# Kernel optimization log

Hardware: AMD Instinct MI355X
Metric: run time of the kernel (lower is better)

Reference implementation:

```python
import jax, jax.numpy as jnp
import numpy as np

DIM = 1024
N_HEADS = 16
HEAD_DIM = DIM // N_HEADS
WINDOW = 64


def setup_inputs() -> dict:
    key = jax.random.key(0)
    k1, k2, k3 = jax.random.split(key, 3)
    B, N = 4, 8192
    x = jax.random.normal(k1, (B, N, DIM), dtype=jnp.float32)
    w_qkv = jax.random.normal(k2, (3 * DIM, DIM), dtype=jnp.float32) * (1.0 / np.sqrt(DIM))
    b_qkv = jnp.zeros((3 * DIM,), dtype=jnp.float32)
    w_proj = jax.random.normal(k3, (DIM, DIM), dtype=jnp.float32) * (1.0 / np.sqrt(DIM))
    b_proj = jnp.zeros((DIM,), dtype=jnp.float32)
    return {"x": x, "w_qkv": w_qkv, "b_qkv": b_qkv, "w_proj": w_proj, "b_proj": b_proj}


def reference(x, w_qkv, b_qkv, w_proj, b_proj):
    B, N, C = x.shape
    H, D, W = N_HEADS, HEAD_DIM, WINDOW
    # qkv projection: torch Linear => x @ W.T + b
    qkv = x @ w_qkv.T + b_qkv                      # [B, N, 3C]
    qkv = qkv.reshape(B, N, 3, H, D).transpose(2, 0, 3, 1, 4)  # [3, B, H, N, D]
    q, k, v = qkv[0], qkv[1], qkv[2]               # each [B, H, N, D]
    n_w = N // W                                    # N chosen divisible by window
    # split sequence into non-overlapping windows (block-diagonal attention)
    qw = q.reshape(B, H, n_w, W, D)
    kw = k.reshape(B, H, n_w, W, D)
    vw = v.reshape(B, H, n_w, W, D)
    scale = 1.0 / np.sqrt(D)
    attn = jnp.einsum('bhnqd,bhnkd->bhnqk', qw, kw) * scale  # [B,H,n_w,W,W]
    attn = jax.nn.softmax(attn, axis=-1)
    out = jnp.einsum('bhnqk,bhnkd->bhnqd', attn, vw)          # [B,H,n_w,W,D]
    out = out.reshape(B, H, N, D).transpose(0, 2, 1, 3).reshape(B, N, C)
    return out @ w_proj.T + b_proj
```

## Files before the change

### kernel.cpp

```cpp
#include <hip/hip_runtime.h>
#include <hip/hip_bf16.h>
#include <cstdint>
#include <cstddef>


typedef __attribute__((ext_vector_type(8))) short short8;
typedef __attribute__((ext_vector_type(4))) float float4v;

static __device__ __forceinline__ void async16(void* lds_p, const void* g) {
  __builtin_amdgcn_global_load_lds((const __attribute__((address_space(1))) void*)g,
                                   (__attribute__((address_space(3))) void*)lds_p,
                                   16, 0, 0);
}

static __device__ __forceinline__ unsigned short f2bf_bits(float x) {
  unsigned int u = __float_as_uint(x);
  unsigned int r = (u + 0x7fffu + ((u >> 16) & 1u)) >> 16;
  return (unsigned short)r;
}

#define S_BARRIER() asm volatile("s_barrier" ::: "memory")
#define WAIT_VM(n)  asm volatile("s_waitcnt vmcnt(" #n ")" ::: "memory")

__global__ __launch_bounds__(256) void cast_f32_to_bf16(
    const float* __restrict__ in, unsigned short* __restrict__ out, int n4) {
  int i = blockIdx.x * 256 + threadIdx.x;
  if (i >= n4) return;
  float4 v = ((const float4*)in)[i];
  ushort4 o;
  o.x = f2bf_bits(v.x); o.y = f2bf_bits(v.y);
  o.z = f2bf_bits(v.z); o.w = f2bf_bits(v.w);
  ((ushort4*)out)[i] = o;
}

template<bool OUT_BF16>
__global__ __launch_bounds__(512, 2) void gemm256(
    const unsigned short* __restrict__ A,
    const unsigned short* __restrict__ B,
    const float* __restrict__ bias,
    void* __restrict__ Cout,
    int M, int N, int K, int ntiles)
{
  extern __shared__ unsigned short lds[];

  const int t    = threadIdx.x;
  const int wave = t >> 6;
  const int lane = t & 63;
  const int lr   = lane & 15;
  const int lq   = lane >> 4;
  const int wm   = wave >> 2;
  const int wn   = wave & 3;

  const int nwg  = gridDim.x;
  const int q8   = nwg >> 3;
  const int wg   = ((int)blockIdx.x & 7) * q8 + ((int)blockIdx.x >> 3);
  const int GM   = 8;
  const int group = wg / (GM * ntiles);
  const int inG   = wg % (GM * ntiles);
  const int bm    = group * GM + (inG % GM);
  const int bn    = inG / GM;

  const int srow = t >> 3;
  const int sswz = ((t & 7) ^ (srow & 7)) << 3;
  const unsigned short* Abase = A + (size_t)(bm * 256 + srow) * K + sswz;
  const unsigned short* Bbase = B + (size_t)(bn * 256 + srow) * K + sswz;
  const int ldsw = wave * 512;

  auto stageA = [&](int kt, int c) {
    async16(lds + (kt & 1) * 16384 + c * 4096 + ldsw,
            Abase + (size_t)(c * 64) * K + kt * 64);
  };
  auto stageB = [&](int kt, int c) {
    async16(lds + 32768 + (kt & 1) * 16384 + c * 4096 + ldsw,
            Bbase + (size_t)(c * 64) * K + kt * 64);
  };

  const int g0 = ((0 + lq) ^ (lr & 7)) << 3;
  const int g1 = ((4 + lq) ^ (lr & 7)) << 3;
  const int arow0 = (wm * 128 + lr) * 64;
  const int brow0 = (wn * 64 + lr) * 64;

  float4v acc[8][4];
  #pragma unroll
  for (int i = 0; i < 8; ++i)
    #pragma unroll
    for (int j = 0; j < 4; ++j) acc[i][j] = (float4v){0.f, 0.f, 0.f, 0.f};

  const int NT = K >> 6;

  #pragma unroll
  for (int c = 0; c < 4; ++c) stageB(0, c);
  #pragma unroll
  for (int c = 0; c < 4; ++c) stageA(0, c);
  #pragma unroll
  for (int c = 0; c < 4; ++c) stageB(1, c);
  WAIT_VM(4);
  S_BARRIER();

  short8 af[4][2], bf[2][2], bf2[2][2];

  for (int kt = 0; kt < NT; ++kt) {
    const int bc = kt & 1;
    int kt1 = kt + 1; if (kt1 == NT) kt1 = 0;
    int kt2 = kt + 2; if (kt2 >= NT) kt2 -= NT;
    const unsigned short* Al = lds + bc * 16384;
    const unsigned short* Bl = lds + 32768 + bc * 16384;

    #pragma unroll
    for (int mf = 0; mf < 4; ++mf) {
      af[mf][0] = *(const short8*)(Al + arow0 + mf * 1024 + g0);
      af[mf][1] = *(const short8*)(Al + arow0 + mf * 1024 + g1);
    }
    #pragma unroll
    for (int nf = 0; nf < 2; ++nf) {
      bf[nf][0] = *(const short8*)(Bl + brow0 + nf * 1024 + g0);
      bf[nf][1] = *(const short8*)(Bl + brow0 + nf * 1024 + g1);
    }
    stageA(kt1, 0); stageA(kt1, 2);
    S_BARRIER();
    __builtin_amdgcn_s_setprio(1);
    #pragma unroll
    for (int mf = 0; mf < 4; ++mf)
      #pragma unroll
      for (int nf = 0; nf < 2; ++nf) {
        acc[mf][nf] = __builtin_amdgcn_mfma_f32_16x16x32_bf16(af[mf][0], bf[nf][0], acc[mf][nf], 0, 0, 0);
        acc[mf][nf] = __builtin_amdgcn_mfma_f32_16x16x32_bf16(af[mf][1], bf[nf][1], acc[mf][nf], 0, 0, 0);
      }
    __builtin_amdgcn_s_setprio(0);
    S_BARRIER();

    #pragma unroll
    for (int nf = 0; nf < 2; ++nf) {
      bf2[nf][0] = *(const short8*)(Bl + brow0 + (2 + nf) * 1024 + g0);
      bf2[nf][1] = *(const short8*)(Bl + brow0 + (2 + nf) * 1024 + g1);
    }
    stageA(kt1, 1); stageA(kt1, 3);
    S_BARRIER();
    __builtin_amdgcn_s_setprio(1);
    #pragma unroll
    for (int mf = 0; mf < 4; ++mf)
      #pragma unroll
      for (int nf = 0; nf < 2; ++nf) {
        acc[mf][2 + nf] = __builtin_amdgcn_mfma_f32_16x16x32_bf16(af[mf][0], bf2[nf][0], acc[mf][2 + nf], 0, 0, 0);
        acc[mf][2 + nf] = __builtin_amdgcn_mfma_f32_16x16x32_bf16(af[mf][1], bf2[nf][1], acc[mf][2 + nf], 0, 0, 0);
      }
    __builtin_amdgcn_s_setprio(0);
    S_BARRIER();

    #pragma unroll
    for (int mf = 0; mf < 4; ++mf) {
      af[mf][0] = *(const short8*)(Al + arow0 + (4 + mf) * 1024 + g0);
      af[mf][1] = *(const short8*)(Al + arow0 + (4 + mf) * 1024 + g1);
    }
    stageB(kt2, 0); stageB(kt2, 1);
    S_BARRIER();
    __builtin_amdgcn_s_setprio(1);
    #pragma unroll
    for (int mf = 0; mf < 4; ++mf)
      #pragma unroll
      for (int nf = 0; nf < 2; ++nf) {
        acc[4 + mf][nf] = __builtin_amdgcn_mfma_f32_16x16x32_bf16(af[mf][0], bf[nf][0], acc[4 + mf][nf], 0, 0, 0);
        acc[4 + mf][nf] = __builtin_amdgcn_mfma_f32_16x16x32_bf16(af[mf][1], bf[nf][1], acc[4 + mf][nf], 0, 0, 0);
      }
    __builtin_amdgcn_s_setprio(0);
    S_BARRIER();

    stageB(kt2, 2); stageB(kt2, 3);
    WAIT_VM(4);
    S_BARRIER();
    __builtin_amdgcn_s_setprio(1);
    #pragma unroll
    for (int mf = 0; mf < 4; ++mf)
      #pragma unroll
      for (int nf = 0; nf < 2; ++nf) {
        acc[4 + mf][2 + nf] = __builtin_amdgcn_mfma_f32_16x16x32_bf16(af[mf][0], bf2[nf][0], acc[4 + mf][2 + nf], 0, 0, 0);
        acc[4 + mf][2 + nf] = __builtin_amdgcn_mfma_f32_16x16x32_bf16(af[mf][1], bf2[nf][1], acc[4 + mf][2 + nf], 0, 0, 0);
      }
    __builtin_amdgcn_s_setprio(0);
    S_BARRIER();
  }

  const int rbase = bm * 256 + wm * 128 + lq * 4;
  const int cbase = bn * 256 + wn * 64 + lr;
  #pragma unroll
  for (int nf = 0; nf < 4; ++nf) {
    const int col = cbase + nf * 16;
    const float bv = bias[col];
    #pragma unroll
    for (int mf = 0; mf < 8; ++mf) {
      const int row = rbase + mf * 16;
      #pragma unroll
      for (int r = 0; r < 4; ++r) {
        float v = acc[mf][nf][r] + bv;
        if (OUT_BF16)
          ((unsigned short*)Cout)[(size_t)(row + r) * N + col] = f2bf_bits(v);
        else
          ((float*)Cout)[(size_t)(row + r) * N + col] = v;
      }
    }
  }
}

__global__ __launch_bounds__(256) void win_attn(
    const unsigned short* __restrict__ qkv,
    unsigned short* __restrict__ out)
{
  __shared__ unsigned short Qs[64 * 64];
  __shared__ unsigned short Ks[64 * 64];
  __shared__ unsigned short Vt[64 * 64];
  __shared__ unsigned short Ps[64 * 64];

  const int t    = threadIdx.x;
  const int wave = t >> 6;
  const int lane = t & 63;
  const int wid  = blockIdx.x;
  const int h    = (wid >> 7) & 15;
  const int b    = wid >> 11;
  const int wi   = wid & 127;
  const int tok0 = b * 8192 + wi * 64;

  const unsigned short* qb = qkv + (size_t)tok0 * 3072 + h * 64;
  const unsigned short* kb = qb + 1024;
  const unsigned short* vb = qb + 2048;

  {
    const int row = t >> 3;
    const int col = (t & 7) << 3;
    unsigned short* Qw = Qs + wave * 512;
    unsigned short* Kw = Ks + wave * 512;
    #pragma unroll
    for (int o = 0; o < 2; ++o) {
      async16(Qw + o * 2048, qb + (size_t)(o * 32 + row) * 3072 + col);
      async16(Kw + o * 2048, kb + (size_t)(o * 32 + row) * 3072 + col);
    }
    const int key = lane;
    const int d0  = wave * 8;
    #pragma unroll
    for (int o = 0; o < 2; ++o) {
      const int d = d0 + o * 32;
      ushort4 r0 = *(const ushort4*)(vb + (size_t)key * 3072 + d);
      ushort4 r1 = *(const ushort4*)(vb + (size_t)key * 3072 + d + 4);
      Vt[(d + 0) * 64 + key] = r0.x; Vt[(d + 1) * 64 + key] = r0.y;
      Vt[(d + 2) * 64 + key] = r0.z; Vt[(d + 3) * 64 + key] = r0.w;
      Vt[(d + 4) * 64 + key] = r1.x; Vt[(d + 5) * 64 + key] = r1.y;
      Vt[(d + 6) * 64 + key] = r1.z; Vt[(d + 7) * 64 + key] = r1.w;
    }
  }
  __syncthreads();

  const int lr = lane & 15;
  const int lq = lane >> 4;

  short8 qa[2];
  #pragma unroll
  for (int k2 = 0; k2 < 2; ++k2)
    qa[k2] = *(const short8*)(Qs + (wave * 16 + lr) * 64 + k2 * 32 + lq * 8);

  float4v s[4];
  #pragma unroll
  for (int jt = 0; jt < 4; ++jt) {
    float4v a = (float4v){0.f, 0.f, 0.f, 0.f};
    #pragma unroll
    for (int k2 = 0; k2 < 2; ++k2) {
      short8 kf = *(const short8*)(Ks + (jt * 16 + lr) * 64 + k2 * 32 + lq * 8);
      a = __builtin_amdgcn_mfma_f32_16x16x32_bf16(qa[k2], kf, a, 0, 0, 0);
    }
    s[jt] = a;
  }

  const float scale = 0.125f;
  float pr[4][4];
  #pragma unroll
  for (int r = 0; r < 4; ++r) {
    float m = s[0][r];
    #pragma unroll
    for (int jt = 1; jt < 4; ++jt) m = fmaxf(m, s[jt][r]);
    #pragma unroll
    for (int off = 1; off < 16; off <<= 1) m = fmaxf(m, __shfl_xor(m, off));
    float sum = 0.f;
    #pragma unroll
    for (int jt = 0; jt < 4; ++jt) {
      float e = __expf((s[jt][r] - m) * scale);
      pr[jt][r] = e; sum += e;
    }
    #pragma unroll
    for (int off = 1; off < 16; off <<= 1) sum += __shfl_xor(sum, off);
    float inv = 1.0f / sum;
    #pragma unroll
    for (int jt = 0; jt < 4; ++jt) pr[jt][r] *= inv;
  }

  #pragma unroll
  for (int jt = 0; jt < 4; ++jt)
    #pragma unroll
    for (int r = 0; r < 4; ++r)
      Ps[(wave * 16 + lq * 4 + r) * 64 + jt * 16 + lr] = f2bf_bits(pr[jt][r]);
  __syncthreads();

  short8 pa[2];
  #pragma unroll
  for (int k2 = 0; k2 < 2; ++k2)
    pa[k2] = *(const short8*)(Ps + (wave * 16 + lr) * 64 + k2 * 32 + lq * 8);

  unsigned short* ob = out + h * 64;
  #pragma unroll
  for (int jd = 0; jd < 4; ++jd) {
    float4v a = (float4v){0.f, 0.f, 0.f, 0.f};
    #pragma unroll
    for (int k2 = 0; k2 < 2; ++k2) {
      short8 vf = *(const short8*)(Vt + (jd * 16 + lr) * 64 + k2 * 32 + lq * 8);
      a = __builtin_amdgcn_mfma_f32_16x16x32_bf16(pa[k2], vf, a, 0, 0, 0);
    }
    #pragma unroll
    for (int r = 0; r < 4; ++r) {
      const int row = wave * 16 + lq * 4 + r;
      ob[(size_t)(tok0 + row) * 1024 + jd * 16 + lr] = f2bf_bits(a[r]);
    }
  }
}

extern "C" void kernel_launch(void* const* d_in, const int* in_sizes, int n_in,
                              void* d_out, int out_size, void* d_ws, size_t ws_size,
                              hipStream_t stream) {
  const float* x      = (const float*)d_in[0];
  const float* w_qkv  = (const float*)d_in[1];
  const float* b_qkv  = (const float*)d_in[2];
  const float* w_proj = (const float*)d_in[3];
  const float* b_proj = (const float*)d_in[4];
  float* outp = (float*)d_out;

  char* ws = (char*)d_ws;
  unsigned short* xb     = (unsigned short*)(ws);
  unsigned short* wqkvb  = (unsigned short*)(ws + 67108864);
  unsigned short* wprojb = (unsigned short*)(ws + 73400320);
  unsigned short* qkvb   = (unsigned short*)(ws + 75497472);
  unsigned short* attnb  = (unsigned short*)(ws + 276824064);

  static int attr_done = 0;
  if (!attr_done) {
    hipFuncSetAttribute(reinterpret_cast<const void*>(&gemm256<true>),
                        hipFuncAttributeMaxDynamicSharedMemorySize, 131072);
    hipFuncSetAttribute(reinterpret_cast<const void*>(&gemm256<false>),
                        hipFuncAttributeMaxDynamicSharedMemorySize, 131072);
    attr_done = 1;
  }

  cast_f32_to_bf16<<<32768, 256, 0, stream>>>(x,      xb,     33554432 / 4);
  cast_f32_to_bf16<<<3072,  256, 0, stream>>>(w_qkv,  wqkvb,  3145728 / 4);
  cast_f32_to_bf16<<<1024,  256, 0, stream>>>(w_proj, wprojb, 1048576 / 4);

  gemm256<true><<<128 * 12, 512, 131072, stream>>>(xb, wqkvb, b_qkv, qkvb,
                                                   32768, 3072, 1024, 12);
  win_attn<<<8192, 256, 0, stream>>>(qkvb, attnb);
  gemm256<false><<<128 * 4, 512, 131072, stream>>>(attnb, wprojb, b_proj, outp,
                                                   32768, 1024, 1024, 4);
}
```

Measured before the change: 602.0 us.

## Pipeline windows per attention block and coalesce bf16 stores via LDS staging

The window-attention kernel now handles four windows per block and double-buffers Q/K/V in LDS, so loads for the next window are issued while the current one is computed. Outputs of both the attention kernel and the bf16 QKV GEMM epilogue are staged through swizzled LDS and written as 16-byte vector stores instead of scattered 2-byte stores. This targets uncoalesced global writes and exposed load latency. In exchange there are fewer blocks, more LDS per block, and extra LDS round trips and barriers.

```diff
diff --git a/kernel.cpp b/kernel.cpp
--- a/kernel.cpp
+++ b/kernel.cpp
@@ -180,142 +180,213 @@
     S_BARRIER();
   }
 
-  const int rbase = bm * 256 + wm * 128 + lq * 4;
-  const int cbase = bn * 256 + wn * 64 + lr;
-  #pragma unroll
-  for (int nf = 0; nf < 4; ++nf) {
-    const int col = cbase + nf * 16;
-    const float bv = bias[col];
-    #pragma unroll
-    for (int mf = 0; mf < 8; ++mf) {
-      const int row = rbase + mf * 16;
-      #pragma unroll
-      for (int r = 0; r < 4; ++r) {
-        float v = acc[mf][nf][r] + bv;
-        if (OUT_BF16)
-          ((unsigned short*)Cout)[(size_t)(row + r) * N + col] = f2bf_bits(v);
-        else
-          ((float*)Cout)[(size_t)(row + r) * N + col] = v;
+  WAIT_VM(0);
+
+  if (OUT_BF16) {
+    unsigned short* Ost = lds + wave * 4096;
+    const int cb = bn * 256 + wn * 64;
+    #pragma unroll
+    for (int p = 0; p < 2; ++p) {
+      #pragma unroll
+      for (int nf = 0; nf < 4; ++nf) {
+        const float bv = bias[cb + nf * 16 + lr];
+        #pragma unroll
+        for (int mh = 0; mh < 4; ++mh)
+          #pragma unroll
+          for (int r = 0; r < 4; ++r) {
+            const int row = mh * 16 + lq * 4 + r;
+            Ost[row * 64 + ((nf * 16 + lr) ^ (lq << 4))] =
+                f2bf_bits(acc[p * 4 + mh][nf][r] + bv);
+          }
+      }
+      #pragma unroll
+      for (int k = 0; k < 8; ++k) {
+        const int cid = k * 64 + lane;
+        const int row = cid >> 3;
+        const int c8  = cid & 7;
+        const int lqr = (row >> 2) & 3;
+        short8 v = *(const short8*)(Ost + row * 64 + ((c8 * 8) ^ (lqr << 4)));
+        const size_t grow = (size_t)(bm * 256 + wm * 128 + p * 64 + row);
+        *(short8*)((unsigned short*)Cout + grow * N + cb + c8 * 8) = v;
+      }
+    }
+  } else {
+    const int rbase = bm * 256 + wm * 128 + lq * 4;
+    const int cbase = bn * 256 + wn * 64 + lr;
+    #pragma unroll
+    for (int nf = 0; nf < 4; ++nf) {
+      const int col = cbase + nf * 16;
+      const float bv = bias[col];
+      #pragma unroll
+      for (int mf = 0; mf < 8; ++mf) {
+        const int row = rbase + mf * 16;
+        #pragma unroll
+        for (int r = 0; r < 4; ++r)
+          ((float*)Cout)[(size_t)(row + r) * N + col] = acc[mf][nf][r] + bv;
       }
     }
   }
 }
+
+#define WPB 4
 
 __global__ __launch_bounds__(256) void win_attn(
     const unsigned short* __restrict__ qkv,
     unsigned short* __restrict__ out)
 {
-  __shared__ unsigned short Qs[64 * 64];
-  __shared__ unsigned short Ks[64 * 64];
-  __shared__ unsigned short Vt[64 * 64];
+  __shared__ unsigned short Qs[2][64 * 64];
+  __shared__ unsigned short Ks[2][64 * 64];
+  __shared__ unsigned short Vt[2][64 * 64];
   __shared__ unsigned short Ps[64 * 64];
 
   const int t    = threadIdx.x;
   const int wave = t >> 6;
   const int lane = t & 63;
-  const int wid  = blockIdx.x;
-  const int h    = (wid >> 7) & 15;
-  const int b    = wid >> 11;
-  const int wi   = wid & 127;
-  const int tok0 = b * 8192 + wi * 64;
-
-  const unsigned short* qb = qkv + (size_t)tok0 * 3072 + h * 64;
-  const unsigned short* kb = qb + 1024;
-  const unsigned short* vb = qb + 2048;
-
-  {
-    const int row = t >> 3;
-    const int col = (t & 7) << 3;
-    unsigned short* Qw = Qs + wave * 512;
-    unsigned short* Kw = Ks + wave * 512;
-    #pragma unroll
-    for (int o = 0; o < 2; ++o) {
-      async16(Qw + o * 2048, qb + (size_t)(o * 32 + row) * 3072 + col);
-      async16(Kw + o * 2048, kb + (size_t)(o * 32 + row) * 3072 + col);
-    }
-    const int key = lane;
-    const int d0  = wave * 8;
-    #pragma unroll
-    for (int o = 0; o < 2; ++o) {
-      const int d = d0 + o * 32;
-      ushort4 r0 = *(const ushort4*)(vb + (size_t)key * 3072 + d);
-      ushort4 r1 = *(const ushort4*)(vb + (size_t)key * 3072 + d + 4);
-      Vt[(d + 0) * 64 + key] = r0.x; Vt[(d + 1) * 64 + key] = r0.y;
-      Vt[(d + 2) * 64 + key] = r0.z; Vt[(d + 3) * 64 + key] = r0.w;
-      Vt[(d + 4) * 64 + key] = r1.x; Vt[(d + 5) * 64 + key] = r1.y;
-      Vt[(d + 6) * 64 + key] = r1.z; Vt[(d + 7) * 64 + key] = r1.w;
-    }
-  }
-  __syncthreads();
-
-  const int lr = lane & 15;
-  const int lq = lane >> 4;
-
-  short8 qa[2];
-  #pragma unroll
-  for (int k2 = 0; k2 < 2; ++k2)
-    qa[k2] = *(const short8*)(Qs + (wave * 16 + lr) * 64 + k2 * 32 + lq * 8);
-
-  float4v s[4];
-  #pragma unroll
-  for (int jt = 0; jt < 4; ++jt) {
-    float4v a = (float4v){0.f, 0.f, 0.f, 0.f};
-    #pragma unroll
-    for (int k2 = 0; k2 < 2; ++k2) {
-      short8 kf = *(const short8*)(Ks + (jt * 16 + lr) * 64 + k2 * 32 + lq * 8);
-      a = __builtin_amdgcn_mfma_f32_16x16x32_bf16(qa[k2], kf, a, 0, 0, 0);
-    }
-    s[jt] = a;
-  }
-
-  const float scale = 0.125f;
-  float pr[4][4];
-  #pragma unroll
-  for (int r = 0; r < 4; ++r) {
-    float m = s[0][r];
-    #pragma unroll
-    for (int jt = 1; jt < 4; ++jt) m = fmaxf(m, s[jt][r]);
-    #pragma unroll
-    for (int off = 1; off < 16; off <<= 1) m = fmaxf(m, __shfl_xor(m, off));
-    float sum = 0.f;
+  const int lr   = lane & 15;
+  const int lq   = lane >> 4;
+  const int gbase = blockIdx.x * WPB;
+
+  const int srow = t >> 3;
+  const int scol = (t & 7) << 3;
+
+  ushort4 vr[2][2];
+
+  for (int i = -1, c = 0; i < WPB; ++i) {
+    const int nxt = c ^ 1;
+    if (i + 1 < WPB) {
+      const int g  = gbase + i + 1;
+      const int b  = g >> 11, h = (g >> 7) & 15, wi = g & 127;
+      const unsigned short* qb =
+          qkv + (size_t)(b * 8192 + wi * 64) * 3072 + h * 64;
+      const unsigned short* kb = qb + 1024;
+      const unsigned short* vb = qb + 2048;
+      const int s = (i + 1) & 1;
+      unsigned short* Qw = Qs[s] + wave * 512;
+      unsigned short* Kw = Ks[s] + wave * 512;
+      #pragma unroll
+      for (int o = 0; o < 2; ++o) {
+        async16(Qw + o * 2048, qb + (size_t)(o * 32 + srow) * 3072 + scol);
+        async16(Kw + o * 2048, kb + (size_t)(o * 32 + srow) * 3072 + scol);
+      }
+      #pragma unroll
+      for (int o = 0; o < 2; ++o) {
+        const int d = wave * 8 + o * 32;
+        vr[o][0] = *(const ushort4*)(vb + (size_t)lane * 3072 + d);
+        vr[o][1] = *(const ushort4*)(vb + (size_t)lane * 3072 + d + 4);
+      }
+    }
+
+    if (i < 0) {
+      #pragma unroll
+      for (int o = 0; o < 2; ++o) {
+        const int d = wave * 8 + o * 32;
+        unsigned short* V = Vt[0];
+        V[(d + 0) * 64 + lane] = vr[o][0].x; V[(d + 1) * 64 + lane] = vr[o][0].y;
+        V[(d + 2) * 64 + lane] = vr[o][0].z; V[(d + 3) * 64 + lane] = vr[o][0].w;
+        V[(d + 4) * 64 + lane] = vr[o][1].x; V[(d + 5) * 64 + lane] = vr[o][1].y;
+        V[(d + 6) * 64 + lane] = vr[o][1].z; V[(d + 7) * 64 + lane] = vr[o][1].w;
+      }
+      __syncthreads();
+      continue;
+    }
+
+    const int g  = gbase + i;
+    const int b  = g >> 11, h = (g >> 7) & 15, wi = g & 127;
+    const int tok0 = b * 8192 + wi * 64;
+
+    short8 qa[2];
+    #pragma unroll
+    for (int k2 = 0; k2 < 2; ++k2)
+      qa[k2] = *(const short8*)(Qs[c] + (wave * 16 + lr) * 64 + k2 * 32 + lq * 8);
+
+    float4v s4[4];
     #pragma unroll
     for (int jt = 0; jt < 4; ++jt) {
-      float e = __expf((s[jt][r] - m) * scale);
-      pr[jt][r] = e; sum += e;
-    }
-    #pragma unroll
-    for (int off = 1; off < 16; off <<= 1) sum += __shfl_xor(sum, off);
-    float inv = 1.0f / sum;
-    #pragma unroll
-    for (int jt = 0; jt < 4; ++jt) pr[jt][r] *= inv;
-  }
-
-  #pragma unroll
-  for (int jt = 0; jt < 4; ++jt)
-    #pragma unroll
-    for (int r = 0; r < 4; ++r)
-      Ps[(wave * 16 + lq * 4 + r) * 64 + jt * 16 + lr] = f2bf_bits(pr[jt][r]);
-  __syncthreads();
-
-  short8 pa[2];
-  #pragma unroll
-  for (int k2 = 0; k2 < 2; ++k2)
-    pa[k2] = *(const short8*)(Ps + (wave * 16 + lr) * 64 + k2 * 32 + lq * 8);
-
-  unsigned short* ob = out + h * 64;
-  #pragma unroll
-  for (int jd = 0; jd < 4; ++jd) {
-    float4v a = (float4v){0.f, 0.f, 0.f, 0.f};
-    #pragma unroll
-    for (int k2 = 0; k2 < 2; ++k2) {
-      short8 vf = *(const short8*)(Vt + (jd * 16 + lr) * 64 + k2 * 32 + lq * 8);
-      a = __builtin_amdgcn_mfma_f32_16x16x32_bf16(pa[k2], vf, a, 0, 0, 0);
-    }
+      float4v a = (float4v){0.f, 0.f, 0.f, 0.f};
+      #pragma unroll
+      for (int k2 = 0; k2 < 2; ++k2) {
+        short8 kf = *(const short8*)(Ks[c] + (jt * 16 + lr) * 64 + k2 * 32 + lq * 8);
+        a = __builtin_amdgcn_mfma_f32_16x16x32_bf16(qa[k2], kf, a, 0, 0, 0);
+      }
+      s4[jt] = a;
+    }
+
+    const float scale = 0.125f;
+    float pr[4][4];
     #pragma unroll
     for (int r = 0; r < 4; ++r) {
-      const int row = wave * 16 + lq * 4 + r;
-      ob[(size_t)(tok0 + row) * 1024 + jd * 16 + lr] = f2bf_bits(a[r]);
-    }
+      float m = s4[0][r];
+      #pragma unroll
+      for (int jt = 1; jt < 4; ++jt) m = fmaxf(m, s4[jt][r]);
+      #pragma unroll
+      for (int off = 1; off < 16; off <<= 1) m = fmaxf(m, __shfl_xor(m, off));
+      float sum = 0.f;
+      #pragma unroll
+      for (int jt = 0; jt < 4; ++jt) {
+        float e = __expf((s4[jt][r] - m) * scale);
+        pr[jt][r] = e; sum += e;
+      }
+      #pragma unroll
+      for (int off = 1; off < 16; off <<= 1) sum += __shfl_xor(sum, off);
+      float inv = 1.0f / sum;
+      #pragma unroll
+      for (int jt = 0; jt < 4; ++jt) pr[jt][r] *= inv;
+    }
+
+    #pragma unroll
+    for (int jt = 0; jt < 4; ++jt)
+      #pragma unroll
+      for (int r = 0; r < 4; ++r)
+        Ps[(wave * 16 + lq * 4 + r) * 64 + jt * 16 + lr] = f2bf_bits(pr[jt][r]);
+    __syncthreads();
+
+    short8 pa[2];
+    #pragma unroll
+    for (int k2 = 0; k2 < 2; ++k2)
+      pa[k2] = *(const short8*)(Ps + (wave * 16 + lr) * 64 + k2 * 32 + lq * 8);
+
+    float4v o4[4];
+    #pragma unroll
+    for (int jd = 0; jd < 4; ++jd) {
+      float4v a = (float4v){0.f, 0.f, 0.f, 0.f};
+      #pragma unroll
+      for (int k2 = 0; k2 < 2; ++k2) {
+        short8 vf = *(const short8*)(Vt[c] + (jd * 16 + lr) * 64 + k2 * 32 + lq * 8);
+        a = __builtin_amdgcn_mfma_f32_16x16x32_bf16(pa[k2], vf, a, 0, 0, 0);
+      }
+      o4[jd] = a;
+    }
+
+    unsigned short* Ost = Ps + wave * 1024;
+    #pragma unroll
+    for (int jd = 0; jd < 4; ++jd)
+      #pragma unroll
+      for (int r = 0; r < 4; ++r)
+        Ost[(lq * 4 + r) * 64 + ((jd * 16 + lr) ^ (lq << 4))] =
+            f2bf_bits(o4[jd][r]);
+    #pragma unroll
+    for (int k = 0; k < 2; ++k) {
+      const int cid = k * 64 + lane;
+      const int row = cid >> 3;
+      const int c8  = cid & 7;
+      const int lqr = (row >> 2) & 3;
+      short8 v = *(const short8*)(Ost + row * 64 + ((c8 * 8) ^ (lqr << 4)));
+      *(short8*)(out + (size_t)(tok0 + wave * 16 + row) * 1024 + h * 64 + c8 * 8) = v;
+    }
+
+    if (i + 1 < WPB) {
+      #pragma unroll
+      for (int o = 0; o < 2; ++o) {
+        const int d = wave * 8 + o * 32;
+        unsigned short* V = Vt[nxt];
+        V[(d + 0) * 64 + lane] = vr[o][0].x; V[(d + 1) * 64 + lane] = vr[o][0].y;
+        V[(d + 2) * 64 + lane] = vr[o][0].z; V[(d + 3) * 64 + lane] = vr[o][0].w;
+        V[(d + 4) * 64 + lane] = vr[o][1].x; V[(d + 5) * 64 + lane] = vr[o][1].y;
+        V[(d + 6) * 64 + lane] = vr[o][1].z; V[(d + 7) * 64 + lane] = vr[o][1].w;
+      }
+    }
+    __syncthreads();
+    c ^= 1;
   }
 }
 
@@ -351,7 +422,7 @@
 
   gemm256<true><<<128 * 12, 512, 131072, stream>>>(xb, wqkvb, b_qkv, qkvb,
                                                    32768, 3072, 1024, 12);
-  win_attn<<<8192, 256, 0, stream>>>(qkvb, attnb);
+  win_attn<<<8192 / WPB, 256, 0, stream>>>(qkvb, attnb);
   gemm256<false><<<128 * 4, 512, 131072, stream>>>(attnb, wprojb, b_proj, outp,
                                                    32768, 1024, 1024, 4);
 }
```

After: 588.1 us. -2.3%, faster.
